# Optimization experiments

Hardware: AMD Instinct MI355X
Metric: run time of the kernel (lower is better)

The kernel has to match this reference:

```python
import jax, jax.numpy as jnp
import numpy as np

NEG_RATIO = 3

def setup_inputs() -> dict:
    key = jax.random.key(0)
    k1, k2, k3, k4 = jax.random.split(key, 4)
    B, P = 32, 131072
    loc_data = jax.random.normal(k1, (B, P, 4), dtype=jnp.float32)
    conf_data = jax.random.normal(k2, (B, P, 2), dtype=jnp.float32)
    loc_t = jax.random.normal(k3, (B, P, 4), dtype=jnp.float32)
    conf_t = jax.random.randint(k4, (B, P), 0, 2, dtype=jnp.int64)
    return {"loc_data": loc_data, "conf_data": conf_data, "loc_t": loc_t, "conf_t": conf_t}


def reference(loc_data, conf_data, loc_t, conf_t):
    B, P, _ = loc_data.shape
    pos = conf_t > 0                                   # [B, P]
    num_pos = pos.sum(axis=1, keepdims=True)           # [B, 1] per-sample positive count
    N = num_pos.sum().astype(loc_data.dtype)           # total positives (scalar)

    # --- localization loss: smooth L1 over positive priors, mean over selected elems ---
    d = jnp.abs(loc_data - loc_t)
    sl1 = jnp.where(d < 1.0, 0.5 * d * d, d - 0.5)     # [B, P, 4]
    posf = pos.astype(loc_data.dtype)
    # F.smooth_l1_loss(mean over N_pos*4 selected elements), then /= N
    loss_loc = jnp.sum(sl1 * posf[:, :, None]) / (N * 4.0)
    loss_loc = loss_loc / N

    # --- hard negative mining via double argsort rank trick ---
    # score = logsumexp(conf) - conf[gt class]; positives zeroed out
    gathered = jnp.take_along_axis(conf_data, conf_t[:, :, None], axis=2)[:, :, 0]
    score = jax.nn.logsumexp(conf_data, axis=2) - gathered      # [B, P]
    score = jnp.where(pos, jnp.zeros((), score.dtype), score)
    idx_rank = jnp.argsort(jnp.argsort(-score, axis=1), axis=1)  # rank in descending order
    num_neg = jnp.minimum(NEG_RATIO * num_pos, P - 1)            # clamp max=P-1 (no min clamp)
    neg = idx_rank < num_neg                                     # [B, P]

    # --- confidence loss: CE over pos|neg priors, mean over selected, then /= N ---
    sel = (pos | neg).astype(conf_data.dtype)                    # [B, P]
    logp = jax.nn.log_softmax(conf_data, axis=2)                 # [B, P, 2]
    ce = -jnp.take_along_axis(logp, conf_t[:, :, None], axis=2)[:, :, 0]
    loss_conf = jnp.sum(ce * sel) / jnp.sum(sel)
    loss_conf = loss_conf / N

    return (loss_loc, loss_conf)
```

## Files before the change

### kernel.cpp

```cpp
#include <hip/hip_runtime.h>
#include <cstdint>

#define BB 32
#define PP 131072
#define NEG_RATIO 3

struct Ws {
  float sum_sl1[BB];
  float sum_ce_all[BB];
  float sum_ce_pos[BB];
  float ce_neg[BB];
  int   num_pos[BB];
};

__device__ __forceinline__ float sl1sum(float4 a, float4 b) {
  float dx = fabsf(a.x - b.x), dy = fabsf(a.y - b.y),
        dz = fabsf(a.z - b.z), dw = fabsf(a.w - b.w);
  float sx = dx < 1.0f ? 0.5f * dx * dx : dx - 0.5f;
  float sy = dy < 1.0f ? 0.5f * dy * dy : dy - 0.5f;
  float sz = dz < 1.0f ? 0.5f * dz * dz : dz - 0.5f;
  float sw = dw < 1.0f ? 0.5f * dw * dw : dw - 0.5f;
  return (sx + sy) + (sz + sw);
}

__device__ __forceinline__ float ce_fast(float c0, float c1, int t) {
  float m = fmaxf(c0, c1);
  float d = fabsf(c0 - c1);
  float lse = m + __logf(1.0f + __expf(-d));
  return lse - (t ? c1 : c0);
}

__device__ __forceinline__ float ce_of(float c0, float c1, int t) {
  float m = fmaxf(c0, c1), mn = fminf(c0, c1);
  float lse = m + log1pf(expf(mn - m));
  return lse - (t ? c1 : c0);
}

__global__ __launch_bounds__(256) void k_main(
    const float4* __restrict__ loc, const float4* __restrict__ conf2,
    const float4* __restrict__ loct, const int4* __restrict__ conft4,
    Ws* __restrict__ ws) {
  const int gtid = blockIdx.x * 256 + threadIdx.x;
  const int batch = blockIdx.x >> 7;
  const int p0 = gtid * 4;

  const float4 l0 = loc[p0 + 0], l1 = loc[p0 + 1], l2 = loc[p0 + 2], l3 = loc[p0 + 3];
  const float4 t0 = loct[p0 + 0], t1 = loct[p0 + 1], t2 = loct[p0 + 2], t3 = loct[p0 + 3];
  const float4 ca = conf2[gtid * 2 + 0];
  const float4 cb = conf2[gtid * 2 + 1];
  const int4   tt = conft4[gtid];

  const float ce0 = ce_fast(ca.x, ca.y, tt.x);
  const float ce1 = ce_fast(ca.z, ca.w, tt.y);
  const float ce2 = ce_fast(cb.x, cb.y, tt.z);
  const float ce3 = ce_fast(cb.z, cb.w, tt.w);

  const float s0 = sl1sum(l0, t0), s1 = sl1sum(l1, t1),
              s2 = sl1sum(l2, t2), s3 = sl1sum(l3, t3);

  const float m0 = tt.x > 0 ? 1.0f : 0.0f, m1 = tt.y > 0 ? 1.0f : 0.0f,
              m2 = tt.z > 0 ? 1.0f : 0.0f, m3 = tt.w > 0 ? 1.0f : 0.0f;

  float a_ce_all = (ce0 + ce1) + (ce2 + ce3);
  float a_ce_pos = (m0 * ce0 + m1 * ce1) + (m2 * ce2 + m3 * ce3);
  float a_sl1    = (m0 * s0 + m1 * s1) + (m2 * s2 + m3 * s3);
  int   a_np     = (tt.x > 0) + (tt.y > 0) + (tt.z > 0) + (tt.w > 0);

#pragma unroll
  for (int off = 32; off; off >>= 1) {
    a_sl1    += __shfl_down(a_sl1, off);
    a_ce_all += __shfl_down(a_ce_all, off);
    a_ce_pos += __shfl_down(a_ce_pos, off);
    a_np     += __shfl_down(a_np, off);
  }

  __shared__ float s1s[4], s2s[4], s3s[4];
  __shared__ int s4s[4];
  const int wave = threadIdx.x >> 6, lane = threadIdx.x & 63;
  if (lane == 0) { s1s[wave] = a_sl1; s2s[wave] = a_ce_all; s3s[wave] = a_ce_pos; s4s[wave] = a_np; }
  __syncthreads();
  if (threadIdx.x == 0) {
    atomicAdd(&ws->sum_sl1[batch],    (s1s[0] + s1s[1]) + (s1s[2] + s1s[3]));
    atomicAdd(&ws->sum_ce_all[batch], (s2s[0] + s2s[1]) + (s2s[2] + s2s[3]));
    atomicAdd(&ws->sum_ce_pos[batch], (s3s[0] + s3s[1]) + (s3s[2] + s3s[3]));
    atomicAdd(&ws->num_pos[batch],     s4s[0] + s4s[1] + s4s[2] + s4s[3]);
  }
}

__global__ __launch_bounds__(256) void k_select(
    const float2* __restrict__ conf, const int* __restrict__ conft,
    Ws* __restrict__ ws) {
  const int b = blockIdx.x;
  const int npos = ws->num_pos[b];
  const long long M = (long long)PP - npos;
  long long k = (long long)NEG_RATIO * npos;
  if (k > PP - 1) k = PP - 1;
  if (k >= M) return;
  if (k <= 0) return;

  const int tid = threadIdx.x;
  const int rowbase = b * PP;

  __shared__ unsigned hist[2048];
  __shared__ unsigned sh_prefix;
  __shared__ long long sh_kk;

  unsigned prefix = 0;
  long long kk = k;
  const int shifts[3] = {21, 10, 0};
  const int widths[3] = {11, 11, 10};

  for (int pass = 0; pass < 3; ++pass) {
    const int shift = shifts[pass], width = widths[pass];
    const unsigned mask = (1u << width) - 1u;
    for (int j = tid; j < 2048; j += 256) hist[j] = 0;
    __syncthreads();
    for (int i = tid; i < PP; i += 256) {
      const float2 c = conf[rowbase + i];
      const int t = conft[rowbase + i];
      const float score = (t > 0) ? 0.0f : ce_of(c.x, c.y, t);
      const unsigned u = __float_as_uint(score);
      const bool match = (pass == 0) || ((u >> (shift + width)) == prefix);
      if (match) atomicAdd(&hist[(u >> shift) & mask], 1u);
    }
    __syncthreads();
    if (tid == 0) {
      long long c = 0;
      int d = (int)mask;
      for (; d >= 0; --d) {
        c += hist[d];
        if (c >= kk) break;
      }
      if (d < 0) d = 0;
      sh_prefix = (prefix << width) | (unsigned)d;
      sh_kk = kk - (c - (long long)hist[d]);
    }
    __syncthreads();
    prefix = sh_prefix;
    kk = sh_kk;
    __syncthreads();
  }

  const unsigned Tbits = prefix;
  double local_ce = 0.0;
  __shared__ unsigned wavecnt[4];
  __shared__ long long s_rt;
  if (tid == 0) s_rt = 0;
  __syncthreads();
  const int lane = tid & 63, wave = tid >> 6;

  for (int basei = 0; basei < PP; basei += 256) {
    const int i = basei + tid;
    const float2 c = conf[rowbase + i];
    const int t = conft[rowbase + i];
    const float ce = ce_of(c.x, c.y, t);
    const float score = (t > 0) ? 0.0f : ce;
    const unsigned u = __float_as_uint(score);
    const bool gt = u > Tbits;
    const bool eq = (u == Tbits);
    const unsigned long long bal = __ballot(eq ? 1 : 0);
    if (lane == 0) wavecnt[wave] = (unsigned)__popcll(bal);
    __syncthreads();
    long long cross = s_rt;
    for (int w = 0; w < wave; ++w) cross += wavecnt[w];
    const long long myord = cross + __popcll(bal & ((1ULL << lane) - 1ULL));
    if (gt || (eq && myord < kk)) local_ce += (double)ce;
    __syncthreads();
    if (tid == 0) s_rt += (long long)wavecnt[0] + wavecnt[1] + wavecnt[2] + wavecnt[3];
    __syncthreads();
  }

#pragma unroll
  for (int off = 32; off; off >>= 1) local_ce += __shfl_down(local_ce, off);
  __shared__ double s_ce[4];
  if (lane == 0) s_ce[wave] = local_ce;
  __syncthreads();
  if (tid == 0) ws->ce_neg[b] = (float)(s_ce[0] + s_ce[1] + s_ce[2] + s_ce[3]);
}

__global__ __launch_bounds__(64) void k_final(const Ws* __restrict__ ws,
                                              float* __restrict__ out) {
  const int tid = threadIdx.x;
  double np_d = 0.0, ce_sel = 0.0, cnt = 0.0, sl1 = 0.0;
  if (tid < BB) {
    const int npos = ws->num_pos[tid];
    const long long M = (long long)PP - npos;
    long long k = (long long)NEG_RATIO * npos;
    if (k > PP - 1) k = PP - 1;
    np_d = (double)npos;
    sl1 = (double)ws->sum_sl1[tid];
    if (k >= M) {
      ce_sel = (double)ws->sum_ce_all[tid];
      cnt = (double)PP;
    } else {
      const long long kc = k > 0 ? k : 0;
      ce_sel = (double)ws->sum_ce_pos[tid] + (double)ws->ce_neg[tid];
      cnt = (double)(npos + kc);
    }
  }
#pragma unroll
  for (int off = 32; off; off >>= 1) {
    np_d   += __shfl_down(np_d, off);
    ce_sel += __shfl_down(ce_sel, off);
    cnt    += __shfl_down(cnt, off);
    sl1    += __shfl_down(sl1, off);
  }
  if (tid == 0) {
    const double N = np_d;
    out[0] = (float)(sl1 / (4.0 * N * N));
    out[1] = (float)(ce_sel / cnt / N);
  }
}

extern "C" void kernel_launch(void* const* d_in, const int* in_sizes, int n_in,
                              void* d_out, int out_size, void* d_ws, size_t ws_size,
                              hipStream_t stream) {
  const float4* loc   = (const float4*)d_in[0];
  const float4* conf2 = (const float4*)d_in[1];
  const float2* conf  = (const float2*)d_in[1];
  const float4* loct  = (const float4*)d_in[2];
  const int*    cnft  = (const int*)d_in[3];
  const int4*   cnft4 = (const int4*)d_in[3];
  Ws* ws = (Ws*)d_ws;

  hipMemsetAsync(d_ws, 0, sizeof(Ws), stream);
  k_main<<<dim3((BB * PP) / 1024), dim3(256), 0, stream>>>(loc, conf2, loct, cnft4, ws);
  k_select<<<dim3(BB), dim3(256), 0, stream>>>(conf, cnft, ws);
  k_final<<<dim3(1), dim3(64), 0, stream>>>(ws, (float*)d_out);
}
```

Baseline: 194.6 us.

## Split main reduction into separate conf and loc kernels with strided coalesced loads

```diff
diff --git a/kernel.cpp b/kernel.cpp
--- a/kernel.cpp
+++ b/kernel.cpp
@@ -4,6 +4,8 @@
 #define BB 32
 #define PP 131072
 #define NEG_RATIO 3
+
+typedef float v4f __attribute__((ext_vector_type(4)));
 
 struct Ws {
   float sum_sl1[BB];
@@ -13,7 +15,7 @@
   int   num_pos[BB];
 };
 
-__device__ __forceinline__ float sl1sum(float4 a, float4 b) {
+__device__ __forceinline__ float sl1sum(v4f a, v4f b) {
   float dx = fabsf(a.x - b.x), dy = fabsf(a.y - b.y),
         dz = fabsf(a.z - b.z), dw = fabsf(a.w - b.w);
   float sx = dx < 1.0f ? 0.5f * dx * dx : dx - 0.5f;
@@ -36,54 +38,85 @@
   return lse - (t ? c1 : c0);
 }
 
-__global__ __launch_bounds__(256) void k_main(
-    const float4* __restrict__ loc, const float4* __restrict__ conf2,
-    const float4* __restrict__ loct, const int4* __restrict__ conft4,
+__global__ __launch_bounds__(256) void k_loc(
+    const v4f* __restrict__ loc, const v4f* __restrict__ loct,
+    const int* __restrict__ tt, Ws* __restrict__ ws) {
+  const int tid = threadIdx.x;
+  const int b = blockIdx.x;
+  const int batch = b >> 7;
+  const int p0 = b * 1024 + tid;
+
+  const v4f l0 = __builtin_nontemporal_load(loc + p0 + 0);
+  const v4f l1 = __builtin_nontemporal_load(loc + p0 + 256);
+  const v4f l2 = __builtin_nontemporal_load(loc + p0 + 512);
+  const v4f l3 = __builtin_nontemporal_load(loc + p0 + 768);
+  const v4f g0 = __builtin_nontemporal_load(loct + p0 + 0);
+  const v4f g1 = __builtin_nontemporal_load(loct + p0 + 256);
+  const v4f g2 = __builtin_nontemporal_load(loct + p0 + 512);
+  const v4f g3 = __builtin_nontemporal_load(loct + p0 + 768);
+  const int t0 = tt[p0 + 0];
+  const int t1 = tt[p0 + 256];
+  const int t2 = tt[p0 + 512];
+  const int t3 = tt[p0 + 768];
+  __builtin_amdgcn_sched_barrier(0);
+
+  const float m0 = t0 > 0 ? 1.0f : 0.0f, m1 = t1 > 0 ? 1.0f : 0.0f,
+              m2 = t2 > 0 ? 1.0f : 0.0f, m3 = t3 > 0 ? 1.0f : 0.0f;
+  float a = (m0 * sl1sum(l0, g0) + m1 * sl1sum(l1, g1)) +
+            (m2 * sl1sum(l2, g2) + m3 * sl1sum(l3, g3));
+
+#pragma unroll
+  for (int off = 32; off; off >>= 1) a += __shfl_down(a, off);
+
+  __shared__ float sred[4];
+  const int wave = tid >> 6, lane = tid & 63;
+  if (lane == 0) sred[wave] = a;
+  __syncthreads();
+  if (tid == 0)
+    atomicAdd(&ws->sum_sl1[batch], (sred[0] + sred[1]) + (sred[2] + sred[3]));
+}
+
+__global__ __launch_bounds__(256) void k_conf(
+    const v4f* __restrict__ conf4, const int2* __restrict__ tt2,
     Ws* __restrict__ ws) {
-  const int gtid = blockIdx.x * 256 + threadIdx.x;
-  const int batch = blockIdx.x >> 7;
-  const int p0 = gtid * 4;
-
-  const float4 l0 = loc[p0 + 0], l1 = loc[p0 + 1], l2 = loc[p0 + 2], l3 = loc[p0 + 3];
-  const float4 t0 = loct[p0 + 0], t1 = loct[p0 + 1], t2 = loct[p0 + 2], t3 = loct[p0 + 3];
-  const float4 ca = conf2[gtid * 2 + 0];
-  const float4 cb = conf2[gtid * 2 + 1];
-  const int4   tt = conft4[gtid];
-
-  const float ce0 = ce_fast(ca.x, ca.y, tt.x);
-  const float ce1 = ce_fast(ca.z, ca.w, tt.y);
-  const float ce2 = ce_fast(cb.x, cb.y, tt.z);
-  const float ce3 = ce_fast(cb.z, cb.w, tt.w);
-
-  const float s0 = sl1sum(l0, t0), s1 = sl1sum(l1, t1),
-              s2 = sl1sum(l2, t2), s3 = sl1sum(l3, t3);
-
-  const float m0 = tt.x > 0 ? 1.0f : 0.0f, m1 = tt.y > 0 ? 1.0f : 0.0f,
-              m2 = tt.z > 0 ? 1.0f : 0.0f, m3 = tt.w > 0 ? 1.0f : 0.0f;
-
-  float a_ce_all = (ce0 + ce1) + (ce2 + ce3);
-  float a_ce_pos = (m0 * ce0 + m1 * ce1) + (m2 * ce2 + m3 * ce3);
-  float a_sl1    = (m0 * s0 + m1 * s1) + (m2 * s2 + m3 * s3);
-  int   a_np     = (tt.x > 0) + (tt.y > 0) + (tt.z > 0) + (tt.w > 0);
+  const int tid = threadIdx.x;
+  const int b = blockIdx.x;
+  const int batch = b >> 7;
+  const int j0 = b * 512 + tid;
+
+  const v4f ca = conf4[j0 + 0];
+  const v4f cb = conf4[j0 + 256];
+  const int2 ta = tt2[j0 + 0];
+  const int2 tb = tt2[j0 + 256];
+  __builtin_amdgcn_sched_barrier(0);
+
+  const float ce0 = ce_fast(ca.x, ca.y, ta.x);
+  const float ce1 = ce_fast(ca.z, ca.w, ta.y);
+  const float ce2 = ce_fast(cb.x, cb.y, tb.x);
+  const float ce3 = ce_fast(cb.z, cb.w, tb.y);
+  const float m0 = ta.x > 0 ? 1.0f : 0.0f, m1 = ta.y > 0 ? 1.0f : 0.0f,
+              m2 = tb.x > 0 ? 1.0f : 0.0f, m3 = tb.y > 0 ? 1.0f : 0.0f;
+
+  float a_all = (ce0 + ce1) + (ce2 + ce3);
+  float a_pos = (m0 * ce0 + m1 * ce1) + (m2 * ce2 + m3 * ce3);
+  int   a_np  = (ta.x > 0) + (ta.y > 0) + (tb.x > 0) + (tb.y > 0);
 
 #pragma unroll
   for (int off = 32; off; off >>= 1) {
-    a_sl1    += __shfl_down(a_sl1, off);
-    a_ce_all += __shfl_down(a_ce_all, off);
-    a_ce_pos += __shfl_down(a_ce_pos, off);
-    a_np     += __shfl_down(a_np, off);
-  }
-
-  __shared__ float s1s[4], s2s[4], s3s[4];
-  __shared__ int s4s[4];
-  const int wave = threadIdx.x >> 6, lane = threadIdx.x & 63;
-  if (lane == 0) { s1s[wave] = a_sl1; s2s[wave] = a_ce_all; s3s[wave] = a_ce_pos; s4s[wave] = a_np; }
-  __syncthreads();
-  if (threadIdx.x == 0) {
-    atomicAdd(&ws->sum_sl1[batch],    (s1s[0] + s1s[1]) + (s1s[2] + s1s[3]));
-    atomicAdd(&ws->sum_ce_all[batch], (s2s[0] + s2s[1]) + (s2s[2] + s2s[3]));
-    atomicAdd(&ws->sum_ce_pos[batch], (s3s[0] + s3s[1]) + (s3s[2] + s3s[3]));
-    atomicAdd(&ws->num_pos[batch],     s4s[0] + s4s[1] + s4s[2] + s4s[3]);
+    a_all += __shfl_down(a_all, off);
+    a_pos += __shfl_down(a_pos, off);
+    a_np  += __shfl_down(a_np, off);
+  }
+
+  __shared__ float s1[4], s2[4];
+  __shared__ int s3[4];
+  const int wave = tid >> 6, lane = tid & 63;
+  if (lane == 0) { s1[wave] = a_all; s2[wave] = a_pos; s3[wave] = a_np; }
+  __syncthreads();
+  if (tid == 0) {
+    atomicAdd(&ws->sum_ce_all[batch], (s1[0] + s1[1]) + (s1[2] + s1[3]));
+    atomicAdd(&ws->sum_ce_pos[batch], (s2[0] + s2[1]) + (s2[2] + s2[3]));
+    atomicAdd(&ws->num_pos[batch],     s3[0] + s3[1] + s3[2] + s3[3]);
   }
 }
 
@@ -215,16 +248,17 @@
 extern "C" void kernel_launch(void* const* d_in, const int* in_sizes, int n_in,
                               void* d_out, int out_size, void* d_ws, size_t ws_size,
                               hipStream_t stream) {
-  const float4* loc   = (const float4*)d_in[0];
-  const float4* conf2 = (const float4*)d_in[1];
+  const v4f*    loc   = (const v4f*)d_in[0];
+  const v4f*    conf4 = (const v4f*)d_in[1];
   const float2* conf  = (const float2*)d_in[1];
-  const float4* loct  = (const float4*)d_in[2];
+  const v4f*    loct  = (const v4f*)d_in[2];
   const int*    cnft  = (const int*)d_in[3];
-  const int4*   cnft4 = (const int4*)d_in[3];
+  const int2*   cnft2 = (const int2*)d_in[3];
   Ws* ws = (Ws*)d_ws;
 
   hipMemsetAsync(d_ws, 0, sizeof(Ws), stream);
-  k_main<<<dim3((BB * PP) / 1024), dim3(256), 0, stream>>>(loc, conf2, loct, cnft4, ws);
+  k_conf<<<dim3((BB * PP) / 1024), dim3(256), 0, stream>>>(conf4, cnft2, ws);
+  k_loc<<<dim3((BB * PP) / 1024), dim3(256), 0, stream>>>(loc, loct, cnft, ws);
   k_select<<<dim3(BB), dim3(256), 0, stream>>>(conf, cnft, ws);
   k_final<<<dim3(1), dim3(64), 0, stream>>>(ws, (float*)d_out);
 }
```

Result: slower. 230.1 us (+18.3%).
